# Performance work log

Hardware: AMD Instinct MI355X
Metric: run time of the kernel (lower is better)

Reference implementation:

```python
import jax, jax.numpy as jnp
import numpy as np

MARGIN = 0.2  # init margin
B, D = 4096, 512


def _pairwise_dist(x):
    # torch.cdist(x, x, p=2): Euclidean distance via Gram matrix
    sq = jnp.sum(x * x, axis=-1)                      # [B]
    gram = x @ x.T                                    # [B, B]
    d2 = jnp.maximum(sq[:, None] + sq[None, :] - 2.0 * gram, 0.0)
    safe = jnp.where(d2 > 0, d2, 1.0)                 # grad-safe sqrt at 0
    return jnp.where(d2 > 0, jnp.sqrt(safe), 0.0)


def setup_inputs() -> dict:
    key = jax.random.key(0)
    k1, k2, k3 = jax.random.split(key, 3)
    anchor = jax.random.normal(k1, (B, D), dtype=jnp.float32)
    positive = jax.random.normal(k2, (B, D), dtype=jnp.float32)
    labels = jax.random.randint(k3, (B,), 0, 64)
    return {"anchor": anchor, "positive": positive, "labels": labels}


def reference(anchor, positive, labels):
    d_ap = jnp.sum((anchor - positive) ** 2, axis=-1)          # [B] squared dist
    pd = _pairwise_dist(anchor)                                 # [B, B] euclidean
    diff_label = labels[None, :] != labels[:, None]             # [B, B]
    inf = jnp.float32(jnp.inf)
    # negatives farther than the positive (note: pd is euclidean, d_ap squared,
    # exactly as in the original code)
    cand = jnp.where(diff_label & (pd > d_ap[:, None]), pd, inf)
    min_larger = jnp.min(cand, axis=1)
    # fallback: min over all different-label negatives
    fallback = jnp.min(jnp.where(diff_label, pd, inf), axis=1)
    d_an = jnp.where(jnp.isfinite(min_larger), min_larger, fallback)
    loss = jnp.maximum(d_ap - d_an + MARGIN, 0.0)
    return jnp.mean(loss)
```

## Files before the change

### kernel.cpp

```cpp
#include <hip/hip_runtime.h>
#include <hip/hip_bf16.h>
#include <cstdint>
#include <cstddef>

constexpr int BN = 4096;
constexpr int DN = 512;
constexpr int NT = BN / 128;
constexpr int NBLK = NT * (NT + 1) / 2;
constexpr float MARGIN = 0.2f;
constexpr uint32_t INF_U = 0x7f800000u;

typedef __attribute__((ext_vector_type(8))) short short8;
typedef __attribute__((ext_vector_type(4))) float float4v;

#define AS1(p) ((const __attribute__((address_space(1))) void*)(p))
#define AS3(p) ((__attribute__((address_space(3))) void*)(p))

__global__ __launch_bounds__(256) void prep_kernel(
    const float* __restrict__ anchor,
    const float* __restrict__ positive,
    uint16_t* __restrict__ Abf,
    float* __restrict__ sqn,
    float* __restrict__ dap,
    uint32_t* __restrict__ min_all,
    uint32_t* __restrict__ min_larger,
    uint32_t* __restrict__ done_count)
{
    const int tid  = threadIdx.x;
    const int wave = tid >> 6;
    const int lane = tid & 63;
    const int row  = blockIdx.x * 4 + wave;

    if (blockIdx.x == 0 && tid == 0) *done_count = 0;

    const float4* arow = (const float4*)(anchor   + (size_t)row * DN);
    const float4* prow = (const float4*)(positive + (size_t)row * DN);

    float4 av0 = arow[lane * 2 + 0], av1 = arow[lane * 2 + 1];
    float4 pv0 = prow[lane * 2 + 0], pv1 = prow[lane * 2 + 1];

    float a[8] = {av0.x, av0.y, av0.z, av0.w, av1.x, av1.y, av1.z, av1.w};
    float p[8] = {pv0.x, pv0.y, pv0.z, pv0.w, pv1.x, pv1.y, pv1.z, pv1.w};

    float s = 0.f, d = 0.f;
    union { uint16_t u[8]; uint4 v; } pk;
    #pragma unroll
    for (int i = 0; i < 8; ++i) {
        s += a[i] * a[i];
        float dx = a[i] - p[i];
        d += dx * dx;
        uint32_t ub = __float_as_uint(a[i]);
        pk.u[i] = (uint16_t)((ub + 0x7fffu + ((ub >> 16) & 1u)) >> 16);
    }

    ((uint4*)(Abf + (size_t)row * DN))[lane] = pk.v;

    #pragma unroll
    for (int off = 32; off; off >>= 1) {
        s += __shfl_xor(s, off);
        d += __shfl_xor(d, off);
    }
    if (lane == 0) {
        sqn[row] = s;
        dap[row] = d;
        min_all[row]    = INF_U;
        min_larger[row] = INF_U;
    }
}

__global__ __launch_bounds__(256) void gram_kernel(
    const uint16_t* __restrict__ Abf,
    const float* __restrict__ sqn,
    const float* __restrict__ dap,
    const int* __restrict__ labels,
    uint32_t* __restrict__ min_all,
    uint32_t* __restrict__ min_larger,
    uint32_t* __restrict__ done_count,
    float* __restrict__ out)
{
    __shared__ uint16_t Abuf[128 * 64];
    __shared__ uint16_t Bbuf[128 * 64];

    int t = blockIdx.x, bi = 0, rem = NT;
    while (t >= rem) { t -= rem; ++bi; --rem; }
    const int bj = bi + t;
    const bool offdiag = (bi != bj);
    const int rowBase = bi * 128;
    const int colBase = bj * 128;

    const int tid  = threadIdx.x;
    const int wave = tid >> 6;
    const int lane = tid & 63;
    const int wi   = wave >> 1;
    const int wj   = wave & 1;
    const int quad = lane >> 4;
    const int l15  = lane & 15;

    const int lrow   = lane >> 3;
    const int lchunk = (lane & 7) ^ lrow;

    float4v acc[4][4];
    #pragma unroll
    for (int i = 0; i < 4; ++i)
        #pragma unroll
        for (int j = 0; j < 4; ++j)
            acc[i][j] = (float4v){0.f, 0.f, 0.f, 0.f};

    for (int kt = 0; kt < DN / 64; ++kt) {
        const int k0 = kt * 64;
        __syncthreads();
        #pragma unroll
        for (int s = 0; s < 4; ++s) {
            const int r0 = (wave * 4 + s) * 8;
            const uint16_t* ga = Abf + (size_t)(rowBase + r0 + lrow) * DN + k0 + lchunk * 8;
            __builtin_amdgcn_global_load_lds(AS1(ga), AS3(Abuf + r0 * 64), 16, 0, 0);
            const uint16_t* gb = Abf + (size_t)(colBase + r0 + lrow) * DN + k0 + lchunk * 8;
            __builtin_amdgcn_global_load_lds(AS1(gb), AS3(Bbuf + r0 * 64), 16, 0, 0);
        }
        __syncthreads();

        #pragma unroll
        for (int kk = 0; kk < 2; ++kk) {
            short8 af[4], bfr[4];
            #pragma unroll
            for (int mi = 0; mi < 4; ++mi) {
                int r = wi * 64 + mi * 16 + l15;
                int p = (kk * 4 + quad) ^ (r & 7);
                af[mi] = *(const short8*)(Abuf + r * 64 + p * 8);
            }
            #pragma unroll
            for (int mj = 0; mj < 4; ++mj) {
                int r = wj * 64 + mj * 16 + l15;
                int p = (kk * 4 + quad) ^ (r & 7);
                bfr[mj] = *(const short8*)(Bbuf + r * 64 + p * 8);
            }
            #pragma unroll
            for (int mi = 0; mi < 4; ++mi)
                #pragma unroll
                for (int mj = 0; mj < 4; ++mj)
                    acc[mi][mj] = __builtin_amdgcn_mfma_f32_16x16x32_bf16(
                        af[mi], bfr[mj], acc[mi][mj], 0, 0, 0);
        }
    }

    const float INFF = __uint_as_float(INF_U);
    float sqj[4], dapj2[4]; int labj[4];
    #pragma unroll
    for (int mj = 0; mj < 4; ++mj) {
        int col = colBase + wj * 64 + mj * 16 + l15;
        sqj[mj]  = sqn[col];
        labj[mj] = labels[col];
        dapj2[mj] = dap[col];
    }
    float cAll[4], cLarger[4];
    #pragma unroll
    for (int mj = 0; mj < 4; ++mj) { cAll[mj] = INFF; cLarger[mj] = INFF; }

    #pragma unroll
    for (int mi = 0; mi < 4; ++mi) {
        #pragma unroll
        for (int r = 0; r < 4; ++r) {
            int row = rowBase + wi * 64 + mi * 16 + quad * 4 + r;
            float sqi   = sqn[row];
            int   li    = labels[row];
            float dapi  = dap[row];
            float mAll = INFF, mLarger = INFF;
            #pragma unroll
            for (int mj = 0; mj < 4; ++mj) {
                float d2 = sqi + sqj[mj] - 2.0f * acc[mi][mj][r];
                d2 = d2 > 0.f ? d2 : 0.f;
                if (labj[mj] != li) {
                    mAll = fminf(mAll, d2);
                    if (d2 > dapi * dapi) mLarger = fminf(mLarger, d2);
                    if (offdiag) {
                        cAll[mj] = fminf(cAll[mj], d2);
                        if (d2 > dapj2[mj] * dapj2[mj]) cLarger[mj] = fminf(cLarger[mj], d2);
                    }
                }
            }
            #pragma unroll
            for (int off = 1; off < 16; off <<= 1) {
                mAll    = fminf(mAll,    __shfl_xor(mAll, off));
                mLarger = fminf(mLarger, __shfl_xor(mLarger, off));
            }
            if (l15 == 0) {
                atomicMin(&min_all[row],    __float_as_uint(mAll));
                atomicMin(&min_larger[row], __float_as_uint(mLarger));
            }
        }
    }
    if (offdiag) {
        #pragma unroll
        for (int mj = 0; mj < 4; ++mj) {
            float a0 = cAll[mj], l0 = cLarger[mj];
            a0 = fminf(a0, __shfl_xor(a0, 16)); l0 = fminf(l0, __shfl_xor(l0, 16));
            a0 = fminf(a0, __shfl_xor(a0, 32)); l0 = fminf(l0, __shfl_xor(l0, 32));
            if (quad == 0) {
                int col = colBase + wj * 64 + mj * 16 + l15;
                atomicMin(&min_all[col],    __float_as_uint(a0));
                atomicMin(&min_larger[col], __float_as_uint(l0));
            }
        }
    }

    __shared__ bool isLast;
    __syncthreads();
    if (tid == 0) {
        __threadfence();
        isLast = (atomicAdd(done_count, 1u) == NBLK - 1);
    }
    __syncthreads();
    if (isLast) {
        __threadfence();
        float s = 0.f;
        for (int i = tid; i < BN; i += 256) {
            uint32_t mlu = __hip_atomic_load(&min_larger[i], __ATOMIC_RELAXED, __HIP_MEMORY_SCOPE_AGENT);
            uint32_t mau = __hip_atomic_load(&min_all[i],    __ATOMIC_RELAXED, __HIP_MEMORY_SCOPE_AGENT);
            float dan2 = (mlu != INF_U) ? __uint_as_float(mlu) : __uint_as_float(mau);
            float l = dap[i] - sqrtf(dan2) + MARGIN;
            s += l > 0.f ? l : 0.f;
        }
        #pragma unroll
        for (int off = 32; off; off >>= 1) s += __shfl_xor(s, off);
        __shared__ float wsum[4];
        if ((tid & 63) == 0) wsum[tid >> 6] = s;
        __syncthreads();
        if (tid == 0) out[0] = (wsum[0] + wsum[1] + wsum[2] + wsum[3]) * (1.0f / BN);
    }
}

extern "C" void kernel_launch(void* const* d_in, const int* in_sizes, int n_in,
                              void* d_out, int out_size, void* d_ws, size_t ws_size,
                              hipStream_t stream) {
    const float* anchor   = (const float*)d_in[0];
    const float* positive = (const float*)d_in[1];
    const int*   labels   = (const int*)d_in[2];
    float* out = (float*)d_out;

    uint8_t* ws = (uint8_t*)d_ws;
    uint16_t* Abf        = (uint16_t*)ws;
    float*    sqn        = (float*)(ws + (size_t)BN * DN * 2);
    float*    dap        = sqn + BN;
    uint32_t* min_all    = (uint32_t*)(dap + BN);
    uint32_t* min_larger = min_all + BN;
    uint32_t* done_count = min_larger + BN;

    prep_kernel<<<BN / 4, 256, 0, stream>>>(anchor, positive, Abf, sqn, dap,
                                            min_all, min_larger, done_count);
    gram_kernel<<<NBLK, 256, 0, stream>>>(Abf, sqn, dap, labels,
                                          min_all, min_larger, done_count, out);
}
```

Baseline: 123.1 us.

## Pack per-row metadata into float4, use register-staged tile loads, add occupancy hint

Per-row squared norm, d_ap, d_ap squared and label are packed into one float4 in the prep kernel, so the gram epilogue does one vector load per row instead of three scalar loads and no longer recomputes the square. The direct global-to-LDS async loads are replaced with register-staged uint4 loads followed by swizzled LDS stores. A launch_bounds minimum of 3 blocks per SM is added. Register staging adds VGPR pressure and a round trip through registers, and the occupancy hint may force spilling.

```diff
diff --git a/kernel.cpp b/kernel.cpp
--- a/kernel.cpp
+++ b/kernel.cpp
@@ -13,15 +13,12 @@
 typedef __attribute__((ext_vector_type(8))) short short8;
 typedef __attribute__((ext_vector_type(4))) float float4v;
 
-#define AS1(p) ((const __attribute__((address_space(1))) void*)(p))
-#define AS3(p) ((__attribute__((address_space(3))) void*)(p))
-
 __global__ __launch_bounds__(256) void prep_kernel(
     const float* __restrict__ anchor,
     const float* __restrict__ positive,
+    const int* __restrict__ labels,
     uint16_t* __restrict__ Abf,
-    float* __restrict__ sqn,
-    float* __restrict__ dap,
+    float4* __restrict__ meta,
     uint32_t* __restrict__ min_all,
     uint32_t* __restrict__ min_larger,
     uint32_t* __restrict__ done_count)
@@ -61,18 +58,15 @@
         d += __shfl_xor(d, off);
     }
     if (lane == 0) {
-        sqn[row] = s;
-        dap[row] = d;
+        meta[row] = (float4){s, d, d * d, __uint_as_float((uint32_t)labels[row])};
         min_all[row]    = INF_U;
         min_larger[row] = INF_U;
     }
 }
 
-__global__ __launch_bounds__(256) void gram_kernel(
+__global__ __launch_bounds__(256, 3) void gram_kernel(
     const uint16_t* __restrict__ Abf,
-    const float* __restrict__ sqn,
-    const float* __restrict__ dap,
-    const int* __restrict__ labels,
+    const float4* __restrict__ meta,
     uint32_t* __restrict__ min_all,
     uint32_t* __restrict__ min_larger,
     uint32_t* __restrict__ done_count,
@@ -96,8 +90,12 @@
     const int quad = lane >> 4;
     const int l15  = lane & 15;
 
-    const int lrow   = lane >> 3;
-    const int lchunk = (lane & 7) ^ lrow;
+    int sr[4], sc[4], sp[4];
+    #pragma unroll
+    for (int i = 0; i < 4; ++i) {
+        int l = tid + i * 256;
+        sr[i] = l >> 3; sc[i] = l & 7; sp[i] = sc[i] ^ (sr[i] & 7);
+    }
 
     float4v acc[4][4];
     #pragma unroll
@@ -109,13 +107,20 @@
     for (int kt = 0; kt < DN / 64; ++kt) {
         const int k0 = kt * 64;
         __syncthreads();
-        #pragma unroll
-        for (int s = 0; s < 4; ++s) {
-            const int r0 = (wave * 4 + s) * 8;
-            const uint16_t* ga = Abf + (size_t)(rowBase + r0 + lrow) * DN + k0 + lchunk * 8;
-            __builtin_amdgcn_global_load_lds(AS1(ga), AS3(Abuf + r0 * 64), 16, 0, 0);
-            const uint16_t* gb = Abf + (size_t)(colBase + r0 + lrow) * DN + k0 + lchunk * 8;
-            __builtin_amdgcn_global_load_lds(AS1(gb), AS3(Bbuf + r0 * 64), 16, 0, 0);
+        {
+            uint4 st[4];
+            #pragma unroll
+            for (int i = 0; i < 4; ++i)
+                st[i] = *(const uint4*)(Abf + (size_t)(rowBase + sr[i]) * DN + k0 + sc[i] * 8);
+            #pragma unroll
+            for (int i = 0; i < 4; ++i)
+                *(uint4*)(Abuf + sr[i] * 64 + sp[i] * 8) = st[i];
+            #pragma unroll
+            for (int i = 0; i < 4; ++i)
+                st[i] = *(const uint4*)(Abf + (size_t)(colBase + sr[i]) * DN + k0 + sc[i] * 8);
+            #pragma unroll
+            for (int i = 0; i < 4; ++i)
+                *(uint4*)(Bbuf + sr[i] * 64 + sp[i] * 8) = st[i];
         }
         __syncthreads();
 
@@ -144,14 +149,11 @@
     }
 
     const float INFF = __uint_as_float(INF_U);
-    float sqj[4], dapj2[4]; int labj[4];
-    #pragma unroll
-    for (int mj = 0; mj < 4; ++mj) {
-        int col = colBase + wj * 64 + mj * 16 + l15;
-        sqj[mj]  = sqn[col];
-        labj[mj] = labels[col];
-        dapj2[mj] = dap[col];
-    }
+    float4 mj_meta[4];
+    #pragma unroll
+    for (int mj = 0; mj < 4; ++mj)
+        mj_meta[mj] = meta[colBase + wj * 64 + mj * 16 + l15];
+
     float cAll[4], cLarger[4];
     #pragma unroll
     for (int mj = 0; mj < 4; ++mj) { cAll[mj] = INFF; cLarger[mj] = INFF; }
@@ -161,20 +163,19 @@
         #pragma unroll
         for (int r = 0; r < 4; ++r) {
             int row = rowBase + wi * 64 + mi * 16 + quad * 4 + r;
-            float sqi   = sqn[row];
-            int   li    = labels[row];
-            float dapi  = dap[row];
+            float4 mim = meta[row];
+            uint32_t li = __float_as_uint(mim.w);
             float mAll = INFF, mLarger = INFF;
             #pragma unroll
             for (int mj = 0; mj < 4; ++mj) {
-                float d2 = sqi + sqj[mj] - 2.0f * acc[mi][mj][r];
+                float d2 = mim.x + mj_meta[mj].x - 2.0f * acc[mi][mj][r];
                 d2 = d2 > 0.f ? d2 : 0.f;
-                if (labj[mj] != li) {
+                if (__float_as_uint(mj_meta[mj].w) != li) {
                     mAll = fminf(mAll, d2);
-                    if (d2 > dapi * dapi) mLarger = fminf(mLarger, d2);
+                    if (d2 > mim.z) mLarger = fminf(mLarger, d2);
                     if (offdiag) {
                         cAll[mj] = fminf(cAll[mj], d2);
-                        if (d2 > dapj2[mj] * dapj2[mj]) cLarger[mj] = fminf(cLarger[mj], d2);
+                        if (d2 > mj_meta[mj].z) cLarger[mj] = fminf(cLarger[mj], d2);
                     }
                 }
             }
@@ -217,7 +218,7 @@
             uint32_t mlu = __hip_atomic_load(&min_larger[i], __ATOMIC_RELAXED, __HIP_MEMORY_SCOPE_AGENT);
             uint32_t mau = __hip_atomic_load(&min_all[i],    __ATOMIC_RELAXED, __HIP_MEMORY_SCOPE_AGENT);
             float dan2 = (mlu != INF_U) ? __uint_as_float(mlu) : __uint_as_float(mau);
-            float l = dap[i] - sqrtf(dan2) + MARGIN;
+            float l = meta[i].y - sqrtf(dan2) + MARGIN;
             s += l > 0.f ? l : 0.f;
         }
         #pragma unroll
@@ -239,14 +240,12 @@
 
     uint8_t* ws = (uint8_t*)d_ws;
     uint16_t* Abf        = (uint16_t*)ws;
-    float*    sqn        = (float*)(ws + (size_t)BN * DN * 2);
-    float*    dap        = sqn + BN;
-    uint32_t* min_all    = (uint32_t*)(dap + BN);
+    float4*   meta       = (float4*)(ws + (size_t)BN * DN * 2);
+    uint32_t* min_all    = (uint32_t*)(meta + BN);
     uint32_t* min_larger = min_all + BN;
     uint32_t* done_count = min_larger + BN;
 
-    prep_kernel<<<BN / 4, 256, 0, stream>>>(anchor, positive, Abf, sqn, dap,
+    prep_kernel<<<BN / 4, 256, 0, stream>>>(anchor, positive, labels, Abf, meta,
                                             min_all, min_larger, done_count);
-    gram_kernel<<<NBLK, 256, 0, stream>>>(Abf, sqn, dap, labels,
-                                          min_all, min_larger, done_count, out);
+    gram_kernel<<<NBLK, 256, 0, stream>>>(Abf, meta, min_all, min_larger, done_count, out);
 }
```

Result: faster. 106.6 us (-13.4%).
